# Kernel optimization log

Measured on AMD Instinct MI355X. Metric: run time of the kernel, lower is better.

## Reference

```python
import jax, jax.numpy as jnp
import numpy as np

B = 2048
NUM_ITER = 3  # dynamic routing iterations


def _conv2d(x, w, b, pad):
    # x: [B,C,H,W], w: [O,I,kh,kw] (OIHW)
    y = jax.lax.conv_general_dilated(
        x, w, window_strides=(1, 1), padding=[(pad, pad), (pad, pad)],
        dimension_numbers=('NCHW', 'OIHW', 'NCHW'))
    return y + b[None, :, None, None]


def _maxpool2(x):
    return jax.lax.reduce_window(x, -jnp.inf, jax.lax.max,
                                 (1, 1, 2, 2), (1, 1, 2, 2), 'VALID')


def _squash(t, axis=-1):
    # scale = |t|^2/(1+|t|^2); out = scale * t / |t|
    n2 = jnp.sum(t * t, axis=axis, keepdims=True)
    return (n2 / (1.0 + n2)) * t * jax.lax.rsqrt(n2)


def setup_inputs() -> dict:
    key = jax.random.key(0)
    ks = jax.random.split(key, 8)
    f32 = jnp.float32
    rn = lambda k, s, sc=1.0: jax.random.normal(k, s, f32) * sc
    return {
        'x': rn(ks[0], (B, 1, 36, 60)),
        'y': rn(ks[1], (B, 2)),
        'conv1_w': rn(ks[2], (20, 1, 5, 5), 0.1),
        'conv1_b': jnp.zeros((20,), f32),
        'conv2_w': rn(ks[3], (50, 20, 5, 5), 0.01),
        'conv2_b': jnp.zeros((50,), f32),
        'pcaps_w': rn(ks[4], (16, 50, 5, 5), 0.05),   # 4 capsules x 4 out-ch, stacked
        'pcaps_b': jnp.zeros((16,), f32),
        'route_w': rn(ks[5], (2, 288, 4, 1)),          # [num_caps, route_nodes, in_ch, out_ch]
        'fc1_w': rn(ks[6], (500, 3602), 0.02),
        'fc1_b': jnp.zeros((500,), f32),
        'fc2_w': rn(ks[7], (2, 502), 0.05),
        'fc2_b': jnp.zeros((2,), f32),
    }


def reference(x, y, conv1_w, conv1_b, conv2_w, conv2_b, pcaps_w, pcaps_b,
              route_w, fc1_w, fc1_b, fc2_w, fc2_b):
    b = x.shape[0]
    # conv backbone
    h = _maxpool2(_conv2d(x, conv1_w, conv1_b, 0))   # [B,20,16,28]
    h = _maxpool2(_conv2d(h, conv2_w, conv2_b, 0))   # [B,50,6,12]

    # primary capsules: 4 parallel convs (stacked into one), each [B,4,6,12]
    p = _conv2d(h, pcaps_w, pcaps_b, 2)              # [B,16,6,12]
    u = p.reshape(b, 4, 4 * 6 * 12)                  # [B, caps=4, nodes=288] (c,h,w flatten per capsule)
    u = u.transpose(0, 2, 1)                         # [B,288,4]
    u = _squash(u, axis=-1)

    # digit capsules: dynamic routing
    # priors[k,b,r,o] = sum_c u[b,r,c] * W[k,r,c,o]
    priors = jnp.einsum('brc,krco->kbro', u, route_w)  # [2,B,288,1]
    logits = jnp.zeros_like(priors)
    v = None
    for i in range(NUM_ITER):
        probs = jax.nn.softmax(logits, axis=2)
        v = _squash(jnp.sum(probs * priors, axis=2, keepdims=True), axis=-1)  # [2,B,1,1]
        if i < NUM_ITER - 1:
            logits = logits + jnp.sum(priors * v, axis=-1, keepdims=True)

    c = v[:, :, 0, :].transpose(1, 0, 2).reshape(b, -1)  # [B,2]
    xf = h.reshape(b, -1)                                # [B,3600]
    f = jnp.concatenate([xf, c], axis=-1)                # [B,3602]
    f = jax.nn.relu(f @ fc1_w.T + fc1_b)                 # [B,500]
    f = jnp.concatenate([f, y], axis=1)                  # [B,502]
    return f @ fc2_w.T + fc2_b                           # [B,2]
```

## Files before the change

kernel.cpp:

```cpp
#include <hip/hip_runtime.h>
#include <math.h>


#define BATCH 2048

typedef __attribute__((ext_vector_type(8))) short short8;
typedef __attribute__((ext_vector_type(4))) float floatx4;
typedef unsigned short u16;
typedef unsigned int   u32;

__device__ inline float wave_sum(float v) {
#pragma unroll
    for (int off = 32; off >= 1; off >>= 1) v += __shfl_xor(v, off);
    return v;
}
__device__ inline float wave_max(float v) {
#pragma unroll
    for (int off = 32; off >= 1; off >>= 1) v = fmaxf(v, __shfl_xor(v, off));
    return v;
}
__device__ inline u16 f2bf(float f) {
    u32 u = __float_as_uint(f);
    u32 r = (u + 0x7FFFu + ((u >> 16) & 1u)) >> 16;
    return (u16)r;
}

__global__ __launch_bounds__(256) void k_prep(
    const float* __restrict__ fw,  u16* __restrict__ w_bf,
    const float* __restrict__ w2,  u16* __restrict__ w2t,
    const float* __restrict__ pcw, u16* __restrict__ w_pc,
    const float* __restrict__ w1,  u16* __restrict__ w1t)
{
    const int blk = blockIdx.x, t = threadIdx.x;
    if (blk < 904) {
        int g  = blk * 256 + t;
        int n  = (g * 8) / 3616;
        int k0 = (g * 8) % 3616;
        u16 v[8];
#pragma unroll
        for (int j = 0; j < 8; ++j) {
            int kk = k0 + j;
            float f = 0.f;
            if (n < 500 && kk < 3600) {
                int pos = kk / 50;
                int oc  = kk - 50 * pos;
                f = fw[(size_t)n * 3602 + oc * 72 + pos];
            }
            v[j] = f2bf(f);
        }
        *(short8*)&w_bf[(size_t)g * 8] = *(short8*)v;
    } else if (blk < 929) {
        int g   = (blk - 904) * 256 + t;
        int idx = g * 8;
        int tap = idx >> 11;
        int oc  = (idx >> 5) & 63;
        int ic0 = idx & 31;
        u16 v[8];
#pragma unroll
        for (int j = 0; j < 8; ++j) {
            int ic = ic0 + j;
            float f = (ic < 20 && oc < 50) ? w2[oc * 500 + ic * 25 + tap] : 0.f;
            v[j] = f2bf(f);
        }
        *(short8*)&w2t[idx] = *(short8*)v;
    } else if (blk < 942) {
        int g = (blk - 929) * 256 + t;
        if (g >= 3200) return;
        int idx = g * 8;
        int tap = idx >> 10;
        int rem = idx & 1023;
        int oc  = rem >> 6;
        int ic0 = rem & 63;
        u16 v[8];
#pragma unroll
        for (int j = 0; j < 8; ++j) {
            int ic = ic0 + j;
            float f = (ic < 50) ? pcw[(oc * 50 + ic) * 25 + tap] : 0.f;
            v[j] = f2bf(f);
        }
        *(short8*)&w_pc[idx] = *(short8*)v;
    } else {
        if (t < 128) {
            int n  = t >> 2;
            int k0 = (t & 3) * 8;
            u16 v[8];
#pragma unroll
            for (int j = 0; j < 8; ++j) {
                int k = k0 + j;
                float f = (n < 20 && k < 25) ? w1[n * 25 + k] : 0.f;
                v[j] = f2bf(f);
            }
            *(short8*)&w1t[t * 8] = *(short8*)v;
        }
    }
}

__global__ __launch_bounds__(256, 3) void k_convs(
    const float* __restrict__ x, const u16* __restrict__ w1t,
    const float* __restrict__ b1, const u16* __restrict__ w2t,
    const float* __restrict__ b2, u32* __restrict__ h_bf)
{
    __shared__ __align__(16) u16 h1t[17920];
    __shared__ __align__(16) u16 xbf[2304];
    __shared__ __align__(16) u16 im2[4480];

    const int t = threadIdx.x;
    const int b = blockIdx.x;

    for (int i = t; i < 2688; i += 256) {
        int pos = i / 6, c = i - 6 * pos;
        ((u32*)h1t)[pos * 20 + 10 + c] = 0u;
    }
    const float* xb = x + b * 2160;
    for (int i = t; i < 2160; i += 256) {
        int r = i / 60, c = i - 60 * r;
        xbf[r * 64 + c] = f2bf(xb[i]);
    }
    __syncthreads();

    const int lane = t & 63, w = t >> 6;
    const int r16  = lane & 15;
    const int q    = lane >> 4;

    short8 w1f[2];
#pragma unroll
    for (int nt = 0; nt < 2; ++nt)
        w1f[nt] = *(const short8*)&w1t[(nt * 16 + r16) * 32 + q * 8];

    const int p_   = t;
    const int px_  = p_ >> 2;
    const int dy_  = (p_ & 3) >> 1, dx_ = p_ & 1;
    const int xc_  = 2 * px_ + dx_;
    const int j0_  = xc_ >> 1;
    const int par_ = xc_ & 1;

#pragma unroll 1
    for (int c = 0; c < 16; ++c) {
        if (t < 112) {
            u16 tap[25];
#pragma unroll
            for (int r = 0; r < 5; ++r) {
                const u32* U = (const u32*)&xbf[(2 * c + dy_ + r) * 64];
                u32 A0 = U[j0_], A1 = U[j0_ + 1], A2 = U[j0_ + 2];
                u16 e0 = par_ ? (u16)(A0 >> 16) : (u16)A0;
                u16 e1 = par_ ? (u16)A1         : (u16)(A0 >> 16);
                u16 e2 = par_ ? (u16)(A1 >> 16) : (u16)A1;
                u16 e3 = par_ ? (u16)A2         : (u16)(A1 >> 16);
                u16 e4 = par_ ? (u16)(A2 >> 16) : (u16)A2;
                tap[r * 5 + 0] = e0; tap[r * 5 + 1] = e1; tap[r * 5 + 2] = e2;
                tap[r * 5 + 3] = e3; tap[r * 5 + 4] = e4;
            }
            u32 ow[16];
#pragma unroll
            for (int j = 0; j < 12; ++j)
                ow[j] = (u32)tap[2 * j] | ((u32)tap[2 * j + 1] << 16);
            ow[12] = (u32)tap[24];
            ow[13] = 0u; ow[14] = 0u; ow[15] = 0u;
            u32* dst = (u32*)&im2[p_ * 40];
            *(uint4*)&dst[0]  = make_uint4(ow[0],  ow[1],  ow[2],  ow[3]);
            *(uint4*)&dst[4]  = make_uint4(ow[4],  ow[5],  ow[6],  ow[7]);
            *(uint4*)&dst[8]  = make_uint4(ow[8],  ow[9],  ow[10], ow[11]);
            *(uint4*)&dst[12] = make_uint4(ow[12], ow[13], ow[14], ow[15]);
        }
        __syncthreads();
#pragma unroll
        for (int mi = 0; mi < 2; ++mi) {
            int mt = w + 4 * mi;
            if (mt < 7) {
                short8 af = *(const short8*)&im2[(mt * 16 + r16) * 40 + q * 8];
                floatx4 a1[2] = {};
#pragma unroll
                for (int nt = 0; nt < 2; ++nt)
                    a1[nt] = __builtin_amdgcn_mfma_f32_16x16x32_bf16(
                        af, w1f[nt], a1[nt], 0, 0, 0);
                int pq = mt * 4 + q;
#pragma unroll
                for (int nt = 0; nt < 2; ++nt) {
                    int oc = nt * 16 + r16;
                    if (oc < 20) {
                        floatx4 a = a1[nt];
                        float v = fmaxf(fmaxf(a[0], a[1]), fmaxf(a[2], a[3]))
                                + b1[oc];
                        h1t[(c * 28 + pq) * 40 + oc] = f2bf(v);
                    }
                }
            }
        }
        __syncthreads();
    }

    int abase[5];
#pragma unroll
    for (int i = 0; i < 5; ++i) {
        int mt = w + 4 * i;
        if (mt < 18) {
            int m  = mt * 16 + r16;
            int pq = m >> 2, sub = m & 3;
            int py = pq / 12, px = pq - py * 12;
            int yy = py * 2 + (sub >> 1);
            int xx = px * 2 + (sub & 1);
            abase[i] = (yy * 28 + xx) * 40 + q * 8;
        } else abase[i] = 0;
    }
    floatx4 acc2[5][4] = {};
    const u16* wtb = w2t + r16 * 32 + q * 8;

    short8 bf[4];
#pragma unroll
    for (int nt = 0; nt < 4; ++nt)
        bf[nt] = *(const short8*)&wtb[nt * 512];

#pragma unroll 1
    for (int tap = 0; tap < 25; ++tap) {
        short8 bfn[4];
        if (tap < 24) {
#pragma unroll
            for (int nt = 0; nt < 4; ++nt)
                bfn[nt] = *(const short8*)&wtb[(tap + 1) * 2048 + nt * 512];
        }
        int r = tap / 5, s = tap - 5 * r;
        int aoff = r * 1120 + s * 40;
#pragma unroll
        for (int i = 0; i < 5; ++i) {
            int mt = w + 4 * i;
            if (mt < 18) {
                short8 af = *(const short8*)&h1t[abase[i] + aoff];
#pragma unroll
                for (int nt = 0; nt < 4; ++nt)
                    acc2[i][nt] = __builtin_amdgcn_mfma_f32_16x16x32_bf16(
                        af, bf[nt], acc2[i][nt], 0, 0, 0);
            }
        }
#pragma unroll
        for (int nt = 0; nt < 4; ++nt) bf[nt] = bfn[nt];
    }
    __syncthreads();

    float* hs2 = (float*)h1t;
#pragma unroll
    for (int i = 0; i < 5; ++i) {
        int mt = w + 4 * i;
        if (mt < 18) {
            int pq = mt * 4 + q;
#pragma unroll
            for (int nt = 0; nt < 4; ++nt) {
                int oc = nt * 16 + r16;
                if (oc < 50) {
                    floatx4 a = acc2[i][nt];
                    float v = fmaxf(fmaxf(a[0], a[1]), fmaxf(a[2], a[3])) + b2[oc];
                    hs2[pq * 50 + oc] = v;
                }
            }
        }
    }
    __syncthreads();
    u32* ho = h_bf + (size_t)b * 1808;
    for (int i = t; i < 1808; i += 256) {
        int i2 = 2 * i;
        u32 lo = (i2 < 3600) ? f2bf(hs2[i2]) : 0u;
        u32 hi = (i2 + 1 < 3600) ? f2bf(hs2[i2 + 1]) : 0u;
        ho[i] = lo | (hi << 16);
    }
}

__global__ __launch_bounds__(256) void k_pcaps(
    const u32* __restrict__ h_bf, const u16* __restrict__ w_pc,
    const float* __restrict__ pcb, const float* __restrict__ rw,
    float* __restrict__ cbuf)
{
    __shared__ __align__(16) u16 hsbuf[12672];
    __shared__ __align__(16) float pri[576];
    const int t = threadIdx.x;
    const int b = blockIdx.x;

    for (int i = t; i < 6336; i += 256) ((u32*)hsbuf)[i] = 0u;
    __syncthreads();
    {
        const u32* hb = h_bf + (size_t)b * 1808;
        for (int i = t; i < 1800; i += 256) {
            u32 v   = hb[i];
            int k2  = 2 * i;
            int pos = k2 / 50;
            int oc  = k2 - 50 * pos;
            int ph  = pos / 12, pw = pos - 12 * ph;
            ((u32*)hsbuf)[((((ph + 2) * 16) + pw + 2) * 72 + oc) >> 1] = v;
        }
    }
    __syncthreads();

    const int lane = t & 63, w = t >> 6;
    const int r16  = lane & 15;
    const int q    = lane >> 4;
    int abase[5];
#pragma unroll
    for (int mt = 0; mt < 5; ++mt) {
        int m  = mt * 16 + r16;
        int ph = m / 12, pw = m - 12 * ph;
        abase[mt] = (ph * 16 + pw) * 72 + q * 8;
    }
    floatx4 acc[5] = {};
    const u16* wp = w_pc + r16 * 64 + q * 8;
    const int ntap = (28 - w) >> 2;
#pragma unroll 1
    for (int tt = 0; tt < ntap; ++tt) {
        int tap = w + 4 * tt;
        short8 b0 = *(const short8*)&wp[tap * 1024];
        short8 b1 = *(const short8*)&wp[tap * 1024 + 32];
        int r = tap / 5, s = tap - 5 * r;
        int aoff = (r * 16 + s) * 72;
#pragma unroll
        for (int mt = 0; mt < 5; ++mt) {
            short8 a0 = *(const short8*)&hsbuf[abase[mt] + aoff];
            short8 a1 = *(const short8*)&hsbuf[abase[mt] + aoff + 32];
            acc[mt] = __builtin_amdgcn_mfma_f32_16x16x32_bf16(a0, b0, acc[mt], 0, 0, 0);
            acc[mt] = __builtin_amdgcn_mfma_f32_16x16x32_bf16(a1, b1, acc[mt], 0, 0, 0);
        }
    }
    __syncthreads();

    float* psum = (float*)hsbuf;
#pragma unroll
    for (int mt = 0; mt < 5; ++mt)
#pragma unroll
        for (int i = 0; i < 4; ++i) {
            int m = mt * 16 + q * 4 + i;
            psum[w * 1280 + m * 16 + r16] = acc[mt][i];
        }
    __syncthreads();

    for (int i = t; i < 1152; i += 256) {
        float s = psum[i] + psum[1280 + i] + psum[2560 + i] + psum[3840 + i]
                + pcb[i & 15];
        psum[i] = s;
    }
    __syncthreads();

    for (int r = t; r < 288; r += 256) {
        int sub = r / 72;
        int pos = r - sub * 72;
        float u0 = psum[pos * 16 + 0  + sub];
        float u1 = psum[pos * 16 + 4  + sub];
        float u2 = psum[pos * 16 + 8  + sub];
        float u3 = psum[pos * 16 + 12 + sub];
        float n2 = u0 * u0 + u1 * u1 + u2 * u2 + u3 * u3;
        float scale = (n2 / (1.0f + n2)) * rsqrtf(n2);
        u0 *= scale; u1 *= scale; u2 *= scale; u3 *= scale;
#pragma unroll
        for (int k = 0; k < 2; ++k) {
            const float4 wv = *(const float4*)&rw[(k * 288 + r) * 4];
            pri[k * 288 + r] = u0 * wv.x + u1 * wv.y + u2 * wv.z + u3 * wv.w;
        }
    }
    __syncthreads();

    if (w < 2) {
        const float* pr = &pri[w * 288];
        float p[5];
        bool  val[5];
#pragma unroll
        for (int j = 0; j < 5; ++j) {
            int r  = j * 64 + lane;
            val[j] = r < 288;
            p[j]   = val[j] ? pr[r] : 0.0f;
        }
        float tot = wave_sum(p[0] + p[1] + p[2] + p[3] + p[4]);
        float s = tot * (1.0f / 288.0f);
        float a = s * fabsf(s) / (1.0f + s * s);
#pragma unroll
        for (int it = 0; it < 2; ++it) {
            float l[5];
            float lm = -INFINITY;
#pragma unroll
            for (int j = 0; j < 5; ++j) {
                l[j] = val[j] ? p[j] * a : -INFINITY;
                lm   = fmaxf(lm, l[j]);
            }
            lm = wave_max(lm);
            float se = 0.f, sp = 0.f;
#pragma unroll
            for (int j = 0; j < 5; ++j) {
                float e = val[j] ? expf(l[j] - lm) : 0.f;
                se += e;
                sp += e * p[j];
            }
            se = wave_sum(se);
            sp = wave_sum(sp);
            float sv = sp / se;
            float v  = sv * fabsf(sv) / (1.0f + sv * sv);
            if (it == 0) a += v;
            else if (lane == 0) cbuf[b * 2 + w] = v;
        }
    }
}

__global__ __launch_bounds__(256) void k_fc1(
    const u16* __restrict__ h_bf, const u16* __restrict__ w_bf,
    const float* __restrict__ cc, const float* __restrict__ w,
    const float* __restrict__ bias, float* __restrict__ f1)
{
    __shared__ __align__(16) u16 As[64 * 40];
    __shared__ __align__(16) u16 Bs[64 * 40];
    const int t  = threadIdx.x;
    const int m0 = blockIdx.x * 64;
    const int n0 = blockIdx.y * 64;
    const int row = t >> 2, c8 = (t & 3) * 8;
    const u16* ha = &h_bf[(size_t)(m0 + row) * 3616 + c8];
    const u16* wa = &w_bf[(size_t)(n0 + row) * 3616 + c8];
    short8 areg = *(const short8*)ha;
    short8 breg = *(const short8*)wa;
    const int lane = t & 63, wv = t >> 6;
    const int r16 = lane & 15, q = lane >> 4;
    const int wr = row * 40 + (t & 3) * 8;
    const int ar = (wv * 16 + r16) * 40 + q * 8;
    const int br = r16 * 40 + q * 8;
    floatx4 acc[4] = {};
#pragma unroll 1
    for (int it = 0; it < 113; ++it) {
        __syncthreads();
        *(short8*)&As[wr] = areg;
        *(short8*)&Bs[wr] = breg;
        __syncthreads();
        if (it < 112) {
            areg = *(const short8*)(ha + (it + 1) * 32);
            breg = *(const short8*)(wa + (it + 1) * 32);
        }
        short8 af = *(const short8*)&As[ar];
#pragma unroll
        for (int nt = 0; nt < 4; ++nt) {
            short8 bfv = *(const short8*)&Bs[nt * 640 + br];
            acc[nt] = __builtin_amdgcn_mfma_f32_16x16x32_bf16(af, bfv, acc[nt], 0, 0, 0);
        }
    }
    const int mbase = m0 + wv * 16 + q * 4;
#pragma unroll
    for (int nt = 0; nt < 4; ++nt) {
        int n = n0 + nt * 16 + r16;
        if (n < 500) {
            float bn  = bias[n];
            float wc0 = w[(size_t)n * 3602 + 3600];
            float wc1 = w[(size_t)n * 3602 + 3601];
#pragma unroll
            for (int i = 0; i < 4; ++i) {
                int m = mbase + i;
                float v = acc[nt][i] + bn + cc[m * 2] * wc0 + cc[m * 2 + 1] * wc1;
                f1[(size_t)m * 500 + n] = fmaxf(v, 0.f);
            }
        }
    }
}

__global__ __launch_bounds__(256) void k_fc2(
    const float* __restrict__ f1, const float* __restrict__ y,
    const float* __restrict__ w, const float* __restrict__ bias,
    float* __restrict__ out)
{
    int wg   = blockIdx.x * 4 + (threadIdx.x >> 6);
    int lane = threadIdx.x & 63;
    int b = wg >> 1, j = wg & 1;
    const float* wj = w + j * 502;
    float acc = 0.f;
    for (int k = lane; k < 500; k += 64) acc += f1[(size_t)b * 500 + k] * wj[k];
    if (lane < 2) acc += y[b * 2 + lane] * wj[500 + lane];
    acc = wave_sum(acc);
    if (lane == 0) out[b * 2 + j] = acc + bias[j];
}

extern "C" void kernel_launch(void* const* d_in, const int* in_sizes, int n_in,
                              void* d_out, int out_size, void* d_ws, size_t ws_size,
                              hipStream_t stream) {
    const float* x    = (const float*)d_in[0];
    const float* y    = (const float*)d_in[1];
    const float* c1w  = (const float*)d_in[2];
    const float* c1b  = (const float*)d_in[3];
    const float* c2w  = (const float*)d_in[4];
    const float* c2b  = (const float*)d_in[5];
    const float* pcw  = (const float*)d_in[6];
    const float* pcb  = (const float*)d_in[7];
    const float* rw   = (const float*)d_in[8];
    const float* f1w  = (const float*)d_in[9];
    const float* f1b  = (const float*)d_in[10];
    const float* f2w  = (const float*)d_in[11];
    const float* f2b  = (const float*)d_in[12];
    float* out = (float*)d_out;

    u32*   h_bf   = (u32*)d_ws;
    u16*   w_bf   = (u16*)(h_bf + (size_t)BATCH * 1808);
    u16*   w2t    = w_bf + (size_t)512 * 3616;
    u16*   w_pc   = w2t + 51200;
    u16*   w1t    = w_pc + 25600;
    float* cbuf   = (float*)(w1t + 1024);
    float* f1     = cbuf + BATCH * 2;

    k_prep<<<943, 256, 0, stream>>>(f1w, w_bf, c2w, w2t, pcw, w_pc, c1w, w1t);
    k_convs<<<BATCH, 256, 0, stream>>>(x, w1t, c1b, w2t, c2b, h_bf);
    k_pcaps<<<BATCH, 256, 0, stream>>>(h_bf, w_pc, pcb, rw, cbuf);
    dim3 g4(32, 8);
    k_fc1<<<g4, 256, 0, stream>>>((const u16*)h_bf, w_bf, cbuf, f1w, f1b, f1);
    k_fc2<<<BATCH * 2 / 4, 256, 0, stream>>>(f1, y, f2w, f2b, out);
}
```

Baseline: 271.1 us.

## Fuse primary capsules into conv kernel and fold fc2 into fc1 epilogue

The primary-capsule and routing stage now runs inside the conv kernel and reuses its shared-memory activations, so the global round trip of h and one launch are gone. fc2 is folded into the fc1 epilogue through shuffle reductions and atomicAdd into the output, which prep pre-initialises with bias plus the y terms. The fc1 weight re-layout now stages each row in shared memory for coalesced reads. Costs: a larger shared-memory footprint and longer conv kernel (possible occupancy loss), and atomics whose float summation order is nondeterministic.

Result: faster. 259.1 us (-4.4%).

```diff
diff --git a/kernel.cpp b/kernel.cpp
--- a/kernel.cpp
+++ b/kernel.cpp
@@ -29,28 +29,34 @@
     const float* __restrict__ fw,  u16* __restrict__ w_bf,
     const float* __restrict__ w2,  u16* __restrict__ w2t,
     const float* __restrict__ pcw, u16* __restrict__ w_pc,
-    const float* __restrict__ w1,  u16* __restrict__ w1t)
+    const float* __restrict__ w1,  u16* __restrict__ w1t,
+    const float* __restrict__ y,   const float* __restrict__ f2w,
+    const float* __restrict__ f2b, float* __restrict__ out)
 {
+    __shared__ __align__(16) float srow[3600];
     const int blk = blockIdx.x, t = threadIdx.x;
-    if (blk < 904) {
-        int g  = blk * 256 + t;
-        int n  = (g * 8) / 3616;
-        int k0 = (g * 8) % 3616;
-        u16 v[8];
-#pragma unroll
-        for (int j = 0; j < 8; ++j) {
-            int kk = k0 + j;
-            float f = 0.f;
-            if (n < 500 && kk < 3600) {
-                int pos = kk / 50;
-                int oc  = kk - 50 * pos;
-                f = fw[(size_t)n * 3602 + oc * 72 + pos];
-            }
-            v[j] = f2bf(f);
-        }
-        *(short8*)&w_bf[(size_t)g * 8] = *(short8*)v;
-    } else if (blk < 929) {
-        int g   = (blk - 904) * 256 + t;
+    if (blk < 500) {
+        const int n = blk;
+        const float* src = fw + (size_t)n * 3602;
+        for (int i = t; i < 1800; i += 256)
+            *(float2*)&srow[2 * i] = *(const float2*)&src[2 * i];
+        __syncthreads();
+        u32* dst = (u32*)(w_bf + (size_t)n * 3616);
+        for (int i = t; i < 1808; i += 256) {
+            int k2 = 2 * i;
+            u32 pk = 0u;
+            if (k2 < 3600) {
+                int pos = k2 / 50, oc = k2 - 50 * pos;
+                pk = (u32)f2bf(srow[oc * 72 + pos])
+                   | ((u32)f2bf(srow[(oc + 1) * 72 + pos]) << 16);
+            }
+            dst[i] = pk;
+        }
+    } else if (blk == 500) {
+        u32* z = (u32*)(w_bf + (size_t)500 * 3616);
+        for (int i = t; i < 21696; i += 256) z[i] = 0u;
+    } else if (blk < 526) {
+        int g   = (blk - 501) * 256 + t;
         int idx = g * 8;
         int tap = idx >> 11;
         int oc  = (idx >> 5) & 63;
@@ -63,8 +69,8 @@
             v[j] = f2bf(f);
         }
         *(short8*)&w2t[idx] = *(short8*)v;
-    } else if (blk < 942) {
-        int g = (blk - 929) * 256 + t;
+    } else if (blk < 539) {
+        int g = (blk - 526) * 256 + t;
         if (g >= 3200) return;
         int idx = g * 8;
         int tap = idx >> 10;
@@ -79,7 +85,7 @@
             v[j] = f2bf(f);
         }
         *(short8*)&w_pc[idx] = *(short8*)v;
-    } else {
+    } else if (blk == 539) {
         if (t < 128) {
             int n  = t >> 2;
             int k0 = (t & 3) * 8;
@@ -92,17 +98,27 @@
             }
             *(short8*)&w1t[t * 8] = *(short8*)v;
         }
+    } else {
+        int b = (blk - 540) * 256 + t;
+        float y0 = y[b * 2], y1 = y[b * 2 + 1];
+        float2 o;
+        o.x = f2b[0] + y0 * f2w[500] + y1 * f2w[501];
+        o.y = f2b[1] + y0 * f2w[502 + 500] + y1 * f2w[502 + 501];
+        *(float2*)&out[b * 2] = o;
     }
 }
 
 __global__ __launch_bounds__(256, 3) void k_convs(
     const float* __restrict__ x, const u16* __restrict__ w1t,
     const float* __restrict__ b1, const u16* __restrict__ w2t,
-    const float* __restrict__ b2, u32* __restrict__ h_bf)
+    const float* __restrict__ b2, const u16* __restrict__ w_pc,
+    const float* __restrict__ pcb, const float* __restrict__ rw,
+    u32* __restrict__ h_bf, float* __restrict__ cbuf)
 {
-    __shared__ __align__(16) u16 h1t[17920];
-    __shared__ __align__(16) u16 xbf[2304];
-    __shared__ __align__(16) u16 im2[4480];
+    __shared__ __align__(16) u16 smem[24704];
+    u16* h1t = smem;
+    u16* xbf = smem + 17920;
+    u16* im2 = smem + 20224;
 
     const int t = threadIdx.x;
     const int b = blockIdx.x;
@@ -236,7 +252,7 @@
     }
     __syncthreads();
 
-    float* hs2 = (float*)h1t;
+    float* hs2 = (float*)smem;
 #pragma unroll
     for (int i = 0; i < 5; ++i) {
         int mt = w + 4 * i;
@@ -253,52 +269,33 @@
             }
         }
     }
-    __syncthreads();
+    for (int i = t; i < 6336; i += 256)
+        ((u32*)smem)[3600 + i] = 0u;
+    __syncthreads();
+
+    u16* hsbuf = smem + 7200;
     u32* ho = h_bf + (size_t)b * 1808;
     for (int i = t; i < 1808; i += 256) {
-        int i2 = 2 * i;
-        u32 lo = (i2 < 3600) ? f2bf(hs2[i2]) : 0u;
-        u32 hi = (i2 + 1 < 3600) ? f2bf(hs2[i2 + 1]) : 0u;
-        ho[i] = lo | (hi << 16);
-    }
-}
-
-__global__ __launch_bounds__(256) void k_pcaps(
-    const u32* __restrict__ h_bf, const u16* __restrict__ w_pc,
-    const float* __restrict__ pcb, const float* __restrict__ rw,
-    float* __restrict__ cbuf)
-{
-    __shared__ __align__(16) u16 hsbuf[12672];
-    __shared__ __align__(16) float pri[576];
-    const int t = threadIdx.x;
-    const int b = blockIdx.x;
-
-    for (int i = t; i < 6336; i += 256) ((u32*)hsbuf)[i] = 0u;
-    __syncthreads();
-    {
-        const u32* hb = h_bf + (size_t)b * 1808;
-        for (int i = t; i < 1800; i += 256) {
-            u32 v   = hb[i];
-            int k2  = 2 * i;
+        if (i < 1800) {
+            int k2 = 2 * i;
+            u32 pk = (u32)f2bf(hs2[k2]) | ((u32)f2bf(hs2[k2 + 1]) << 16);
+            ho[i] = pk;
             int pos = k2 / 50;
             int oc  = k2 - 50 * pos;
             int ph  = pos / 12, pw = pos - 12 * ph;
-            ((u32*)hsbuf)[((((ph + 2) * 16) + pw + 2) * 72 + oc) >> 1] = v;
-        }
-    }
-    __syncthreads();
-
-    const int lane = t & 63, w = t >> 6;
-    const int r16  = lane & 15;
-    const int q    = lane >> 4;
-    int abase[5];
+            ((u32*)hsbuf)[((((ph + 2) * 16) + pw + 2) * 72 + oc) >> 1] = pk;
+        } else ho[i] = 0u;
+    }
+    __syncthreads();
+
+    int pbase[5];
 #pragma unroll
     for (int mt = 0; mt < 5; ++mt) {
         int m  = mt * 16 + r16;
         int ph = m / 12, pw = m - 12 * ph;
-        abase[mt] = (ph * 16 + pw) * 72 + q * 8;
-    }
-    floatx4 acc[5] = {};
+        pbase[mt] = (ph * 16 + pw) * 72 + q * 8;
+    }
+    floatx4 pacc[5] = {};
     const u16* wp = w_pc + r16 * 64 + q * 8;
     const int ntap = (28 - w) >> 2;
 #pragma unroll 1
@@ -310,21 +307,21 @@
         int aoff = (r * 16 + s) * 72;
 #pragma unroll
         for (int mt = 0; mt < 5; ++mt) {
-            short8 a0 = *(const short8*)&hsbuf[abase[mt] + aoff];
-            short8 a1 = *(const short8*)&hsbuf[abase[mt] + aoff + 32];
-            acc[mt] = __builtin_amdgcn_mfma_f32_16x16x32_bf16(a0, b0, acc[mt], 0, 0, 0);
-            acc[mt] = __builtin_amdgcn_mfma_f32_16x16x32_bf16(a1, b1, acc[mt], 0, 0, 0);
-        }
-    }
-    __syncthreads();
-
-    float* psum = (float*)hsbuf;
+            short8 a0 = *(const short8*)&hsbuf[pbase[mt] + aoff];
+            short8 a1 = *(const short8*)&hsbuf[pbase[mt] + aoff + 32];
+            pacc[mt] = __builtin_amdgcn_mfma_f32_16x16x32_bf16(a0, b0, pacc[mt], 0, 0, 0);
+            pacc[mt] = __builtin_amdgcn_mfma_f32_16x16x32_bf16(a1, b1, pacc[mt], 0, 0, 0);
+        }
+    }
+    __syncthreads();
+
+    float* psum = (float*)(smem + 7200);
 #pragma unroll
     for (int mt = 0; mt < 5; ++mt)
 #pragma unroll
         for (int i = 0; i < 4; ++i) {
             int m = mt * 16 + q * 4 + i;
-            psum[w * 1280 + m * 16 + r16] = acc[mt][i];
+            psum[w * 1280 + m * 16 + r16] = pacc[mt][i];
         }
     __syncthreads();
 
@@ -335,6 +332,7 @@
     }
     __syncthreads();
 
+    float* pri = (float*)(smem + 19872);
     for (int r = t; r < 288; r += 256) {
         int sub = r / 72;
         int pos = r - sub * 72;
@@ -396,7 +394,8 @@
 __global__ __launch_bounds__(256) void k_fc1(
     const u16* __restrict__ h_bf, const u16* __restrict__ w_bf,
     const float* __restrict__ cc, const float* __restrict__ w,
-    const float* __restrict__ bias, float* __restrict__ f1)
+    const float* __restrict__ bias, const float* __restrict__ f2w,
+    float* __restrict__ out)
 {
     __shared__ __align__(16) u16 As[64 * 40];
     __shared__ __align__(16) u16 Bs[64 * 40];
@@ -432,6 +431,8 @@
         }
     }
     const int mbase = m0 + wv * 16 + q * 4;
+    float s0[4] = {0.f, 0.f, 0.f, 0.f};
+    float s1[4] = {0.f, 0.f, 0.f, 0.f};
 #pragma unroll
     for (int nt = 0; nt < 4; ++nt) {
         int n = n0 + nt * 16 + r16;
@@ -439,30 +440,32 @@
             float bn  = bias[n];
             float wc0 = w[(size_t)n * 3602 + 3600];
             float wc1 = w[(size_t)n * 3602 + 3601];
+            float w20 = f2w[n];
+            float w21 = f2w[502 + n];
 #pragma unroll
             for (int i = 0; i < 4; ++i) {
                 int m = mbase + i;
-                float v = acc[nt][i] + bn + cc[m * 2] * wc0 + cc[m * 2 + 1] * wc1;
-                f1[(size_t)m * 500 + n] = fmaxf(v, 0.f);
-            }
-        }
-    }
-}
-
-__global__ __launch_bounds__(256) void k_fc2(
-    const float* __restrict__ f1, const float* __restrict__ y,
-    const float* __restrict__ w, const float* __restrict__ bias,
-    float* __restrict__ out)
-{
-    int wg   = blockIdx.x * 4 + (threadIdx.x >> 6);
-    int lane = threadIdx.x & 63;
-    int b = wg >> 1, j = wg & 1;
-    const float* wj = w + j * 502;
-    float acc = 0.f;
-    for (int k = lane; k < 500; k += 64) acc += f1[(size_t)b * 500 + k] * wj[k];
-    if (lane < 2) acc += y[b * 2 + lane] * wj[500 + lane];
-    acc = wave_sum(acc);
-    if (lane == 0) out[b * 2 + j] = acc + bias[j];
+                float v = fmaxf(acc[nt][i] + bn + cc[m * 2] * wc0
+                                + cc[m * 2 + 1] * wc1, 0.f);
+                s0[i] += v * w20;
+                s1[i] += v * w21;
+            }
+        }
+    }
+#pragma unroll
+    for (int i = 0; i < 4; ++i) {
+        float a0 = s0[i], a1 = s1[i];
+#pragma unroll
+        for (int off = 1; off <= 8; off <<= 1) {
+            a0 += __shfl_xor(a0, off);
+            a1 += __shfl_xor(a1, off);
+        }
+        if (r16 == 0) {
+            int m = mbase + i;
+            atomicAdd(&out[m * 2], a0);
+            atomicAdd(&out[m * 2 + 1], a1);
+        }
+    }
 }
 
 extern "C" void kernel_launch(void* const* d_in, const int* in_sizes, int n_in,
@@ -483,18 +486,18 @@
     const float* f2b  = (const float*)d_in[12];
     float* out = (float*)d_out;
 
-    u32*   h_bf   = (u32*)d_ws;
-    u16*   w_bf   = (u16*)(h_bf + (size_t)BATCH * 1808);
-    u16*   w2t    = w_bf + (size_t)512 * 3616;
-    u16*   w_pc   = w2t + 51200;
-    u16*   w1t    = w_pc + 25600;
-    float* cbuf   = (float*)(w1t + 1024);
-    float* f1     = cbuf + BATCH * 2;
-
-    k_prep<<<943, 256, 0, stream>>>(f1w, w_bf, c2w, w2t, pcw, w_pc, c1w, w1t);
-    k_convs<<<BATCH, 256, 0, stream>>>(x, w1t, c1b, w2t, c2b, h_bf);
-    k_pcaps<<<BATCH, 256, 0, stream>>>(h_bf, w_pc, pcb, rw, cbuf);
+    u32*   h_bf = (u32*)d_ws;
+    u16*   w_bf = (u16*)(h_bf + (size_t)BATCH * 1808);
+    u16*   w2t  = w_bf + (size_t)512 * 3616;
+    u16*   w_pc = w2t + 51200;
+    u16*   w1t  = w_pc + 25600;
+    float* cbuf = (float*)(w1t + 1024);
+
+    k_prep<<<548, 256, 0, stream>>>(f1w, w_bf, c2w, w2t, pcw, w_pc, c1w, w1t,
+                                    y, f2w, f2b, out);
+    k_convs<<<BATCH, 256, 0, stream>>>(x, w1t, c1b, w2t, c2b, w_pc, pcb, rw,
+                                       h_bf, cbuf);
     dim3 g4(32, 8);
-    k_fc1<<<g4, 256, 0, stream>>>((const u16*)h_bf, w_bf, cbuf, f1w, f1b, f1);
-    k_fc2<<<BATCH * 2 / 4, 256, 0, stream>>>(f1, y, f2w, f2b, out);
-}
+    k_fc1<<<g4, 256, 0, stream>>>((const u16*)h_bf, w_bf, cbuf, f1w, f1b,
+                                  f2w, out);
+}
```
